# Kernel optimization log

Hardware: AMD Instinct MI355X
Metric: run time of the kernel (lower is better)

## Reference

```python
import jax, jax.numpy as jnp
import numpy as np
import math

N_HEADS = 12
HEAD_DIM = 64
D_MODEL = 768
BATCH = 2
SEQ = 2048
GRID = 46  # num_patches_per_side


def _rope_1d(x, pos, dim):
    # x: (B,S,H,dim), pos: (S,) int -> rotary embedding along last dim
    inv_freq = 1.0 / (10000.0 ** (jnp.arange(0, dim, 2, dtype=jnp.float32) / dim))  # (dim/2,)
    ang = pos.astype(jnp.float32)[:, None] * inv_freq  # (S, dim/2)
    cos = jnp.concatenate([jnp.cos(ang), jnp.cos(ang)], axis=-1)[None, :, None, :]
    sin = jnp.concatenate([jnp.sin(ang), jnp.sin(ang)], axis=-1)[None, :, None, :]
    x1, x2 = jnp.split(x, 2, axis=-1)
    rot = jnp.concatenate([-x2, x1], axis=-1)
    return x * cos.astype(x.dtype) + rot * sin.astype(x.dtype)


def _rope_2d(x, row_ids, col_ids):
    # 2D RoPE: first half of head_dim rotated by row position, second half by column position
    half = x.shape[-1] // 2
    xr = _rope_1d(x[..., :half], row_ids, half)
    xc = _rope_1d(x[..., half:], col_ids, half)
    return jnp.concatenate([xr, xc], axis=-1)


def setup_inputs() -> dict:
    key = jax.random.key(0)
    ks = jax.random.split(key, 7)
    scale = 1.0 / math.sqrt(D_MODEL)
    return {
        "x": jax.random.normal(ks[0], (BATCH, SEQ, D_MODEL), dtype=jnp.float32),
        "row_ids": jax.random.randint(ks[1], (SEQ,), 0, GRID),
        "col_ids": jax.random.randint(ks[2], (SEQ,), 0, GRID),
        "Wq": jax.random.normal(ks[3], (D_MODEL, D_MODEL), dtype=jnp.float32) * scale,
        "Wk": jax.random.normal(ks[4], (D_MODEL, D_MODEL), dtype=jnp.float32) * scale,
        "Wv": jax.random.normal(ks[5], (D_MODEL, D_MODEL), dtype=jnp.float32) * scale,
        "Wo": jax.random.normal(ks[6], (D_MODEL, D_MODEL), dtype=jnp.float32) * scale,
    }


def reference(x, row_ids, col_ids, Wq, Wk, Wv, Wo):
    B, S, _ = x.shape
    # projections (nn.Linear: y = x @ W.T)
    q = (x @ Wq.T).reshape(B, S, N_HEADS, HEAD_DIM)
    k = (x @ Wk.T).reshape(B, S, N_HEADS, HEAD_DIM)
    v = (x @ Wv.T).reshape(B, S, N_HEADS, HEAD_DIM)
    q = _rope_2d(q, row_ids, col_ids)
    k = _rope_2d(k, row_ids, col_ids)
    # (B,H,S,D)
    q = q.transpose(0, 2, 1, 3)
    k = k.transpose(0, 2, 1, 3)
    v = v.transpose(0, 2, 1, 3)
    scale = 1.0 / math.sqrt(HEAD_DIM)
    scores = jnp.einsum('bhqd,bhkd->bhqk', q, k) * scale  # (B,H,S,S)
    causal = jnp.triu(jnp.ones((S, S), dtype=bool), k=1)
    scores = jnp.where(causal, -jnp.inf, scores)
    attn = jax.nn.softmax(scores, axis=-1)
    out = jnp.einsum('bhqk,bhkd->bhqd', attn, v)
    out = out.transpose(0, 2, 1, 3).reshape(B, S, D_MODEL)
    return out @ Wo.T
```

## Files before the change

### kernel.cpp

```cpp
#include <hip/hip_runtime.h>
#include <stdint.h>
#include <stddef.h>

#define DEV __device__ __forceinline__

typedef unsigned short u16;
typedef __attribute__((ext_vector_type(8))) __bf16 bf16x8;
typedef __attribute__((ext_vector_type(4))) float f32x4;
typedef __attribute__((ext_vector_type(8))) unsigned short u16x8;
typedef __attribute__((ext_vector_type(4))) unsigned short u16x4;

DEV u16 f2bf(float f) {
  uint32_t u = __builtin_bit_cast(uint32_t, f);
  u += 0x7fffu + ((u >> 16) & 1u);
  return (u16)(u >> 16);
}
DEV float bf2f(u16 h) {
  uint32_t u = ((uint32_t)h) << 16;
  return __builtin_bit_cast(float, u);
}
DEV f32x4 mfma16(bf16x8 a, bf16x8 b, f32x4 c) {
  return __builtin_amdgcn_mfma_f32_16x16x32_bf16(a, b, c, 0, 0, 0);
}
DEV void ld_lds16(const void* g, void* l) {
  __builtin_amdgcn_global_load_lds((const __attribute__((address_space(1))) void*)g,
                                   (__attribute__((address_space(3))) void*)l, 16, 0, 0);
}

__global__ __launch_bounds__(256) void k_cvt_all(const float* __restrict__ x,
                                                 const float* __restrict__ wq,
                                                 const float* __restrict__ wk,
                                                 const float* __restrict__ wv,
                                                 const float* __restrict__ wo,
                                                 u16* __restrict__ dx,
                                                 u16* __restrict__ dqkv,
                                                 u16* __restrict__ dwo) {
  const int bid = blockIdx.x;
  const float* src;
  u16* dst;
  int off;
  if (bid < 3072) {
    src = x; dst = dx; off = bid;
  } else {
    const int t = bid - 3072;
    const int w = t / 576;
    off = t - w * 576;
    src = (w == 0) ? wq : (w == 1) ? wk : (w == 2) ? wv : wo;
    dst = (w < 3) ? (dqkv + (size_t)w * 589824) : dwo;
  }
  const int i = (off * 256 + threadIdx.x) * 4;
  const float4 f = *(const float4*)(src + i);
  u16x4 o;
  o.x = f2bf(f.x); o.y = f2bf(f.y); o.z = f2bf(f.z); o.w = f2bf(f.w);
  *(u16x4*)(dst + i) = o;
}

template <bool OUT_F32>
__global__ __launch_bounds__(256) void k_gemm_bt(const u16* __restrict__ A,
                                                 const u16* __restrict__ B,
                                                 void* __restrict__ Cv,
                                                 int N, int K) {
  __shared__ __align__(16) u16 sA[128 * 64];
  __shared__ __align__(16) u16 sB[128 * 64];
  const int tid = threadIdx.x;
  const int lane = tid & 63;
  const int wid = tid >> 6;
  const int wm = wid & 1, wn = wid >> 1;
  const int col16 = lane & 15, quad = lane >> 4;
  const int rowBase = blockIdx.y * 128;
  const int colBase = blockIdx.x * 128;
  const int seg_r = lane >> 3;
  const int seg_c = lane & 7;

  f32x4 zero; zero[0] = zero[1] = zero[2] = zero[3] = 0.0f;
  f32x4 acc[4][4];
#pragma unroll
  for (int i = 0; i < 4; ++i)
#pragma unroll
    for (int j = 0; j < 4; ++j) acc[i][j] = zero;

  for (int k0 = 0; k0 < K; k0 += 64) {
#pragma unroll
    for (int c = 0; c < 4; ++c) {
      const int seg = wid * 4 + c;
      ld_lds16(A + (size_t)(rowBase + seg * 8 + seg_r) * K + k0 + seg_c * 8, sA + seg * 512);
      ld_lds16(B + (size_t)(colBase + seg * 8 + seg_r) * K + k0 + seg_c * 8, sB + seg * 512);
    }
    __syncthreads();
#pragma unroll
    for (int kk = 0; kk < 2; ++kk) {
      bf16x8 af[4], bfr[4];
#pragma unroll
      for (int t = 0; t < 4; ++t) {
        af[t]  = *(const bf16x8*)(sA + (wm * 64 + t * 16 + col16) * 64 + kk * 32 + quad * 8);
        bfr[t] = *(const bf16x8*)(sB + (wn * 64 + t * 16 + col16) * 64 + kk * 32 + quad * 8);
      }
#pragma unroll
      for (int tm = 0; tm < 4; ++tm)
#pragma unroll
        for (int tn = 0; tn < 4; ++tn)
          acc[tm][tn] = mfma16(af[tm], bfr[tn], acc[tm][tn]);
    }
    __syncthreads();
  }

#pragma unroll
  for (int tm = 0; tm < 4; ++tm)
#pragma unroll
    for (int tn = 0; tn < 4; ++tn)
#pragma unroll
      for (int r = 0; r < 4; ++r) {
        const int row = rowBase + wm * 64 + tm * 16 + quad * 4 + r;
        const int col = colBase + wn * 64 + tn * 16 + col16;
        const float v = acc[tm][tn][r];
        if (OUT_F32) ((float*)Cv)[(size_t)row * N + col] = v;
        else         ((u16*)Cv)[(size_t)row * N + col] = f2bf(v);
      }
}

__global__ __launch_bounds__(256, 3) void k_gemm_o(const u16* __restrict__ A,
                                                   const u16* __restrict__ B,
                                                   float* __restrict__ C,
                                                   int N, int K) {
  __shared__ __align__(16) u16 sA[64 * 72];
  __shared__ __align__(16) u16 sB[64 * 72];
  const int tid = threadIdx.x;
  const int lane = tid & 63;
  const int wid = tid >> 6;
  const int col16 = lane & 15, quad = lane >> 4;
  const int wm = wid & 1, wn = wid >> 1;
  const int rowBase = blockIdx.y * 64;
  const int colBase = blockIdx.x * 64;
  const int sr = tid >> 3;
  const int sc8 = (tid & 7) * 8;

  f32x4 zero; zero[0] = zero[1] = zero[2] = zero[3] = 0.0f;
  f32x4 acc[2][2];
  acc[0][0] = zero; acc[0][1] = zero; acc[1][0] = zero; acc[1][1] = zero;

  u16x8 ar[2], br[2];
  auto gload = [&](int k0) {
    ar[0] = *(const u16x8*)(A + (size_t)(rowBase + sr) * K + k0 + sc8);
    ar[1] = *(const u16x8*)(A + (size_t)(rowBase + 32 + sr) * K + k0 + sc8);
    br[0] = *(const u16x8*)(B + (size_t)(colBase + sr) * K + k0 + sc8);
    br[1] = *(const u16x8*)(B + (size_t)(colBase + 32 + sr) * K + k0 + sc8);
  };

  gload(0);
  for (int k0 = 0; k0 < K; k0 += 64) {
    __syncthreads();
    *(u16x8*)&sA[sr * 72 + sc8] = ar[0];
    *(u16x8*)&sA[(32 + sr) * 72 + sc8] = ar[1];
    *(u16x8*)&sB[sr * 72 + sc8] = br[0];
    *(u16x8*)&sB[(32 + sr) * 72 + sc8] = br[1];
    if (k0 + 64 < K) gload(k0 + 64);
    __syncthreads();
#pragma unroll
    for (int kk = 0; kk < 2; ++kk) {
      bf16x8 af[2], bfr[2];
#pragma unroll
      for (int t = 0; t < 2; ++t) {
        af[t]  = *(const bf16x8*)&sA[(wm * 32 + t * 16 + col16) * 72 + kk * 32 + quad * 8];
        bfr[t] = *(const bf16x8*)&sB[(wn * 32 + t * 16 + col16) * 72 + kk * 32 + quad * 8];
      }
#pragma unroll
      for (int tm = 0; tm < 2; ++tm)
#pragma unroll
        for (int tn = 0; tn < 2; ++tn)
          acc[tm][tn] = mfma16(af[tm], bfr[tn], acc[tm][tn]);
    }
  }

#pragma unroll
  for (int tm = 0; tm < 2; ++tm)
#pragma unroll
    for (int tn = 0; tn < 2; ++tn)
#pragma unroll
      for (int r = 0; r < 4; ++r) {
        const int row = rowBase + wm * 32 + tm * 16 + quad * 4 + r;
        const int col = colBase + wn * 32 + tn * 16 + col16;
        C[(size_t)row * N + col] = acc[tm][tn][r];
      }
}

__global__ __launch_bounds__(256) void k_rope_vtrans(const u16* __restrict__ QKV,
                                                     const int* __restrict__ row_ids,
                                                     const int* __restrict__ col_ids,
                                                     u16* __restrict__ Qh,
                                                     u16* __restrict__ Kh,
                                                     u16* __restrict__ Vt) {
  __shared__ __align__(16) u16 tile[64][72];
  if (blockIdx.x < 6144) {
    const int t = blockIdx.x * 256 + threadIdx.x;
    const int p = t & 31;
    const int rest = t >> 5;
    const int h = rest % 12;
    const int bs = rest / 12;
    const int s = bs & 2047;
    const int b = bs >> 11;
    const int f = p & 15;
    const int hs = p >> 4;
    const int pos = hs ? col_ids[s] : row_ids[s];
    const float ang = (float)pos * expf(-(float)f * 0.5756462732485114f);
    float sn, cs;
    sincosf(ang, &sn, &cs);
    const int d1 = hs * 32 + f;
    const int d2 = d1 + 16;
    const size_t ibase = (size_t)bs * 2304 + h * 64;
    const size_t obase = (((size_t)b * 12 + h) * 2048 + s) * 64;
    {
      const float x1 = bf2f(QKV[ibase + d1]);
      const float x2 = bf2f(QKV[ibase + d2]);
      Qh[obase + d1] = f2bf(x1 * cs - x2 * sn);
      Qh[obase + d2] = f2bf(x2 * cs + x1 * sn);
    }
    {
      const float x1 = bf2f(QKV[ibase + 768 + d1]);
      const float x2 = bf2f(QKV[ibase + 768 + d2]);
      Kh[obase + d1] = f2bf(x1 * cs - x2 * sn);
      Kh[obase + d2] = f2bf(x2 * cs + x1 * sn);
    }
  } else {
    const int vb = blockIdx.x - 6144;
    const int s0 = (vb & 31) * 64;
    const int bh = vb >> 5;
    const int b = bh / 12, h = bh % 12;
    const int tid = threadIdx.x;
    const int rl = tid >> 2;
    const int cb = (tid & 3) * 16;
    const u16* src = QKV + ((size_t)b * 2048 + s0 + rl) * 2304 + 1536 + h * 64 + cb;
    const u16x8 v0 = *(const u16x8*)src;
    const u16x8 v1 = *(const u16x8*)(src + 8);
    *(u16x8*)&tile[rl][cb] = v0;
    *(u16x8*)&tile[rl][cb + 8] = v1;
    __syncthreads();
    u16x8 o0, o1;
#pragma unroll
    for (int j = 0; j < 8; ++j) {
      o0[j] = tile[cb + j][rl];
      o1[j] = tile[cb + 8 + j][rl];
    }
    u16* dst = Vt + ((size_t)bh * 64 + rl) * 2048 + s0 + cb;
    *(u16x8*)dst = o0;
    *(u16x8*)(dst + 8) = o1;
  }
}

__global__ __launch_bounds__(256, 3) void k_attn(const u16* __restrict__ Qh,
                                                 const u16* __restrict__ Kh,
                                                 const u16* __restrict__ Vt,
                                                 u16* __restrict__ O,
                                                 u16* __restrict__ Opart,
                                                 float* __restrict__ ml) {
  __shared__ __align__(16) u16 sK[2][64 * 72];
  __shared__ __align__(16) u16 sV[2][64 * 72];
  __shared__ __align__(16) u16 sP[4][16 * 72];
  const int tid = threadIdx.x;
  const int lane = tid & 63;
  const int wid = tid >> 6;
  const int col16 = lane & 15;
  const int quad = lane >> 4;
  const int bx = blockIdx.x;
  const int bh = bx / 80;
  const int u = bx - bh * 80;
  int qt, c;
  if (u < 8)       { qt = u; c = 0; }
  else if (u < 24) { const int t = u - 8;  qt = 8 + (t >> 1); c = t & 1; }
  else if (u < 48) { const int t = u - 24; const int q3 = t / 3; qt = 16 + q3; c = t - q3 * 3; }
  else             { const int t = u - 48; qt = 24 + (t >> 2); c = t & 3; }
  const int nc = (qt >> 3) + 1;
  const int tile0 = c * 8;
  const int tileE = min(tile0 + 8, qt + 1);
  const int ntiles = tileE - tile0;
  const int b = bh / 12, h = bh % 12;
  const int qw = qt * 64 + wid * 16;

  const u16* Qb = Qh + (size_t)bh * (2048 * 64);
  const u16* Kb = Kh + (size_t)bh * (2048 * 64);
  const u16* Vb = Vt + (size_t)bh * (64 * 2048);

  const bf16x8 bQ0 = *(const bf16x8*)(Qb + (size_t)(qw + col16) * 64 + quad * 8);
  const bf16x8 bQ1 = *(const bf16x8*)(Qb + (size_t)(qw + col16) * 64 + 32 + quad * 8);

  f32x4 zero; zero[0] = zero[1] = zero[2] = zero[3] = 0.0f;
  f32x4 o[4];
#pragma unroll
  for (int i = 0; i < 4; ++i) o[i] = zero;
  float m_r = -1e30f, l_r = 0.0f;

  u16* sPw = &sP[wid][0];

  const int sr = tid >> 3;
  const int sc8 = (tid & 7) * 8;
  u16x8 kr[2], vr[2];
  auto gload = [&](int kt) {
#pragma unroll
    for (int i = 0; i < 2; ++i) {
      kr[i] = *(const u16x8*)(Kb + (size_t)(kt + sr + i * 32) * 64 + sc8);
      vr[i] = *(const u16x8*)(Vb + (size_t)(sr + i * 32) * 2048 + kt + sc8);
    }
  };
  auto lwrite = [&](int buf) {
#pragma unroll
    for (int i = 0; i < 2; ++i) {
      *(u16x8*)&sK[buf][(sr + i * 32) * 72 + sc8] = kr[i];
      *(u16x8*)&sV[buf][(sr + i * 32) * 72 + sc8] = vr[i];
    }
  };

  gload(tile0 * 64);
  lwrite(0);
  if (ntiles > 1) gload((tile0 + 1) * 64);
  __syncthreads();

  for (int ki = 0; ki < ntiles; ++ki) {
    const int buf = ki & 1;
    const int kt = (tile0 + ki) * 64;
    if (ki + 1 < ntiles) {
      lwrite(buf ^ 1);
      if (ki + 2 < ntiles) gload((tile0 + ki + 2) * 64);
    }
    bf16x8 ka0[4], ka1[4];
#pragma unroll
    for (int tn = 0; tn < 4; ++tn) {
      const int base = (tn * 16 + col16) * 72 + quad * 8;
      ka0[tn] = *(const bf16x8*)&sK[buf][base];
      ka1[tn] = *(const bf16x8*)&sK[buf][base + 32];
    }
    f32x4 sc[4];
#pragma unroll
    for (int tn = 0; tn < 4; ++tn)
      sc[tn] = mfma16(ka1[tn], bQ1, mfma16(ka0[tn], bQ0, zero));
    bf16x8 va0[4], va1[4];
#pragma unroll
    for (int tn = 0; tn < 4; ++tn) {
      const int base = (tn * 16 + col16) * 72 + quad * 8;
      va0[tn] = *(const bf16x8*)&sV[buf][base];
      va1[tn] = *(const bf16x8*)&sV[buf][base + 32];
    }
    if (kt + 63 > qw) {
#pragma unroll
      for (int tn = 0; tn < 4; ++tn)
#pragma unroll
        for (int rr = 0; rr < 4; ++rr) {
          float v = sc[tn][rr] * 0.125f;
          if (kt + tn * 16 + quad * 4 + rr > qw + col16) v = -1e30f;
          sc[tn][rr] = v;
        }
    } else {
#pragma unroll
      for (int tn = 0; tn < 4; ++tn)
#pragma unroll
        for (int rr = 0; rr < 4; ++rr) sc[tn][rr] *= 0.125f;
    }
    float vm = sc[0][0];
#pragma unroll
    for (int tn = 0; tn < 4; ++tn)
#pragma unroll
      for (int rr = 0; rr < 4; ++rr) vm = fmaxf(vm, sc[tn][rr]);
    vm = fmaxf(vm, __shfl_xor(vm, 16, 64));
    vm = fmaxf(vm, __shfl_xor(vm, 32, 64));
    const float mn = fmaxf(m_r, vm);
    const float alpha = __expf(m_r - mn);
    m_r = mn;
    float rs = 0.0f;
#pragma unroll
    for (int tn = 0; tn < 4; ++tn)
#pragma unroll
      for (int h2 = 0; h2 < 2; ++h2) {
        const float p0 = __expf(sc[tn][2 * h2] - mn);
        const float p1 = __expf(sc[tn][2 * h2 + 1] - mn);
        rs += p0 + p1;
        const uint32_t w = (uint32_t)f2bf(p0) | ((uint32_t)f2bf(p1) << 16);
        ((uint32_t*)sPw)[col16 * 36 + tn * 8 + quad * 2 + h2] = w;
      }
    rs += __shfl_xor(rs, 16, 64);
    rs += __shfl_xor(rs, 32, 64);
    l_r = l_r * alpha + rs;
#pragma unroll
    for (int t = 0; t < 4; ++t)
#pragma unroll
      for (int rr = 0; rr < 4; ++rr) o[t][rr] *= alpha;
    asm volatile("s_waitcnt lgkmcnt(0)" ::: "memory");
    const bf16x8 bP0 = *(const bf16x8*)(sPw + col16 * 72 + quad * 8);
    const bf16x8 bP1 = *(const bf16x8*)(sPw + col16 * 72 + 32 + quad * 8);
#pragma unroll
    for (int tn = 0; tn < 4; ++tn)
      o[tn] = mfma16(va1[tn], bP1, mfma16(va0[tn], bP0, o[tn]));
    __syncthreads();
  }

  if (nc == 1) {
    const float invl = 1.0f / l_r;
    const size_t row = (size_t)b * 2048 + qw + col16;
#pragma unroll
    for (int tn = 0; tn < 4; ++tn)
#pragma unroll
      for (int h2 = 0; h2 < 2; ++h2) {
        const float v0 = o[tn][2 * h2] * invl;
        const float v1 = o[tn][2 * h2 + 1] * invl;
        const uint32_t w = (uint32_t)f2bf(v0) | ((uint32_t)f2bf(v1) << 16);
        const int col = h * 64 + tn * 16 + quad * 4 + 2 * h2;
        *(uint32_t*)(O + row * 768 + col) = w;
      }
  } else {
    u16* op = Opart + (size_t)bx * 4096 + (wid * 16 + col16) * 64;
#pragma unroll
    for (int tn = 0; tn < 4; ++tn)
#pragma unroll
      for (int h2 = 0; h2 < 2; ++h2) {
        const uint32_t w = (uint32_t)f2bf(o[tn][2 * h2]) | ((uint32_t)f2bf(o[tn][2 * h2 + 1]) << 16);
        *(uint32_t*)(op + tn * 16 + quad * 4 + 2 * h2) = w;
      }
    if (quad == 0) {
      float* mlp = ml + (size_t)bx * 128;
      mlp[wid * 16 + col16] = m_r;
      mlp[64 + wid * 16 + col16] = l_r;
    }
  }
}

__global__ __launch_bounds__(256) void k_combine(const u16* __restrict__ Opart,
                                                 const float* __restrict__ ml,
                                                 u16* __restrict__ O) {
  const int bx = blockIdx.x;
  const int bh = bx / 24;
  const int qt = 8 + (bx - bh * 24);
  const int b = bh / 12, h = bh % 12;
  const int nc = (qt >> 3) + 1;
  const int prefix = (qt < 16) ? (8 + 2 * (qt - 8))
                   : (qt < 24) ? (24 + 3 * (qt - 16))
                               : (48 + 4 * (qt - 24));
  const int slot0 = bh * 80 + prefix;
  const int tid = threadIdx.x;
  const int r = tid >> 2;
  const int d0 = (tid & 3) * 16;

  float m_i[4], w_i[4];
  float M = -1e30f;
  for (int i = 0; i < nc; ++i) {
    m_i[i] = ml[(size_t)(slot0 + i) * 128 + r];
    M = fmaxf(M, m_i[i]);
  }
  float l = 0.0f;
  for (int i = 0; i < nc; ++i) {
    w_i[i] = __expf(m_i[i] - M);
    l += w_i[i] * ml[(size_t)(slot0 + i) * 128 + 64 + r];
  }
  const float invl = 1.0f / l;

  float a[16];
#pragma unroll
  for (int j = 0; j < 16; ++j) a[j] = 0.0f;
  for (int i = 0; i < nc; ++i) {
    const u16* op = Opart + (size_t)(slot0 + i) * 4096 + r * 64 + d0;
    const u16x8 v0 = *(const u16x8*)op;
    const u16x8 v1 = *(const u16x8*)(op + 8);
#pragma unroll
    for (int j = 0; j < 8; ++j) {
      a[j] += w_i[i] * bf2f(v0[j]);
      a[8 + j] += w_i[i] * bf2f(v1[j]);
    }
  }
  u16x8 o0, o1;
#pragma unroll
  for (int j = 0; j < 8; ++j) {
    o0[j] = f2bf(a[j] * invl);
    o1[j] = f2bf(a[8 + j] * invl);
  }
  u16* dst = O + (size_t)(b * 2048 + qt * 64 + r) * 768 + h * 64 + d0;
  *(u16x8*)dst = o0;
  *(u16x8*)(dst + 8) = o1;
}

extern "C" void kernel_launch(void* const* d_in, const int* in_sizes, int n_in,
                              void* d_out, int out_size, void* d_ws, size_t ws_size,
                              hipStream_t stream) {
  const float* x       = (const float*)d_in[0];
  const int*   row_ids = (const int*)d_in[1];
  const int*   col_ids = (const int*)d_in[2];
  const float* Wq      = (const float*)d_in[3];
  const float* Wk      = (const float*)d_in[4];
  const float* Wv      = (const float*)d_in[5];
  const float* Wo      = (const float*)d_in[6];
  float* out = (float*)d_out;

  uint8_t* w8 = (uint8_t*)d_ws;
  u16* x_bf = (u16*)(w8 + 0);
  u16* wqkv = (u16*)(w8 + 6291456);
  u16* wo   = (u16*)(w8 + 9830400);
  u16* qkv  = (u16*)(w8 + 11010048);
  u16* qh   = (u16*)(w8 + 29884416);
  u16* kh   = (u16*)(w8 + 36175872);
  u16* vt   = (u16*)(w8 + 42467328);
  u16* obuf = (u16*)(w8 + 48758784);
  u16*   opart = (u16*)(w8 + 11010048);
  float* mlbuf = (float*)(w8 + 11010048 + 15728640);

  k_cvt_all<<<5376, 256, 0, stream>>>(x, Wq, Wk, Wv, Wo, x_bf, wqkv, wo);
  k_gemm_bt<false><<<dim3(18, 32), 256, 0, stream>>>(x_bf, wqkv, (void*)qkv, 2304, 768);
  k_rope_vtrans<<<6912, 256, 0, stream>>>(qkv, row_ids, col_ids, qh, kh, vt);
  k_attn<<<1920, 256, 0, stream>>>(qh, kh, vt, obuf, opart, mlbuf);
  k_combine<<<576, 256, 0, stream>>>(opart, mlbuf, obuf);
  k_gemm_o<<<dim3(12, 64), 256, 0, stream>>>(obuf, wo, out, 768, 768);
}
```

Measured before the change: 190.0 us.

## Fuse RoPE and V transpose into QKV GEMM epilogue, fold softmax scale into Q

The QKV projection GEMM now applies 2D RoPE in its epilogue and writes Q and K directly in head-major layout, with V written transposed. This removes the intermediate QKV buffer and the separate rope/transpose kernel launch. Q is pre-scaled by 1/sqrt(d)*log2(e), so attention uses exp2 and drops the per-score multiply. Probabilities are truncated to bf16 rather than rounded, and the row sum is taken over the truncated values. The costs are more scattered 16-bit stores in the epilogue and a small change in rounding behaviour.

```diff
diff --git a/kernel.cpp b/kernel.cpp
--- a/kernel.cpp
+++ b/kernel.cpp
@@ -26,6 +26,8 @@
   __builtin_amdgcn_global_load_lds((const __attribute__((address_space(1))) void*)g,
                                    (__attribute__((address_space(3))) void*)l, 16, 0, 0);
 }
+
+#define Q_SCALE 0.18033688011112042f
 
 __global__ __launch_bounds__(256) void k_cvt_all(const float* __restrict__ x,
                                                  const float* __restrict__ wq,
@@ -55,13 +57,17 @@
   *(u16x4*)(dst + i) = o;
 }
 
-template <bool OUT_F32>
-__global__ __launch_bounds__(256) void k_gemm_bt(const u16* __restrict__ A,
-                                                 const u16* __restrict__ B,
-                                                 void* __restrict__ Cv,
-                                                 int N, int K) {
+__global__ __launch_bounds__(256) void k_gemm_qkv(const u16* __restrict__ A,
+                                                  const u16* __restrict__ B,
+                                                  const int* __restrict__ row_ids,
+                                                  const int* __restrict__ col_ids,
+                                                  u16* __restrict__ Qh,
+                                                  u16* __restrict__ Kh,
+                                                  u16* __restrict__ Vt) {
+  const int K = 768;
   __shared__ __align__(16) u16 sA[128 * 64];
   __shared__ __align__(16) u16 sB[128 * 64];
+  __shared__ int sIds[256];
   const int tid = threadIdx.x;
   const int lane = tid & 63;
   const int wid = tid >> 6;
@@ -104,18 +110,52 @@
     __syncthreads();
   }
 
-#pragma unroll
-  for (int tm = 0; tm < 4; ++tm)
-#pragma unroll
-    for (int tn = 0; tn < 4; ++tn)
+  const int bx = blockIdx.x;
+  const int type = bx / 6;
+  const int h = (bx % 6) * 2 + wn;
+  const int bb = rowBase >> 11;
+  const int s0 = rowBase & 2047;
+  const size_t bh = (size_t)bb * 12 + h;
+
+  if (type < 2) {
+    if (tid < 128) {
+      sIds[tid] = row_ids[s0 + tid];
+      sIds[128 + tid] = col_ids[s0 + tid];
+    }
+    __syncthreads();
+    u16* dst = (type == 0) ? Qh : Kh;
+    const float scl = (type == 0) ? Q_SCALE : 1.0f;
+    const float invf = exp2f(-(float)col16 * 0.8304820237218406f);
+#pragma unroll
+    for (int tm = 0; tm < 4; ++tm)
 #pragma unroll
       for (int r = 0; r < 4; ++r) {
-        const int row = rowBase + wm * 64 + tm * 16 + quad * 4 + r;
-        const int col = colBase + wn * 64 + tn * 16 + col16;
-        const float v = acc[tm][tn][r];
-        if (OUT_F32) ((float*)Cv)[(size_t)row * N + col] = v;
-        else         ((u16*)Cv)[(size_t)row * N + col] = f2bf(v);
-      }
+        const int lrow = wm * 64 + tm * 16 + quad * 4 + r;
+        const float aR = (float)sIds[lrow] * invf;
+        const float aC = (float)sIds[128 + lrow] * invf;
+        const float cR = __cosf(aR), sR = __sinf(aR);
+        const float cC = __cosf(aC), sC = __sinf(aC);
+        const float x1 = acc[tm][0][r], x2 = acc[tm][1][r];
+        const float x3 = acc[tm][2][r], x4 = acc[tm][3][r];
+        u16* p = dst + (bh * 2048 + s0 + lrow) * 64;
+        p[col16]      = f2bf((x1 * cR - x2 * sR) * scl);
+        p[col16 + 16] = f2bf((x2 * cR + x1 * sR) * scl);
+        p[col16 + 32] = f2bf((x3 * cC - x4 * sC) * scl);
+        p[col16 + 48] = f2bf((x4 * cC + x3 * sC) * scl);
+      }
+  } else {
+#pragma unroll
+    for (int tm = 0; tm < 4; ++tm)
+#pragma unroll
+      for (int tn = 0; tn < 4; ++tn) {
+        const int d = tn * 16 + col16;
+        const int srow = s0 + wm * 64 + tm * 16 + quad * 4;
+        u16x4 o4;
+#pragma unroll
+        for (int r = 0; r < 4; ++r) o4[r] = f2bf(acc[tm][tn][r]);
+        *(u16x4*)(Vt + (bh * 64 + d) * 2048 + srow) = o4;
+      }
+  }
 }
 
 __global__ __launch_bounds__(256, 3) void k_gemm_o(const u16* __restrict__ A,
@@ -181,69 +221,6 @@
         const int col = colBase + wn * 32 + tn * 16 + col16;
         C[(size_t)row * N + col] = acc[tm][tn][r];
       }
-}
-
-__global__ __launch_bounds__(256) void k_rope_vtrans(const u16* __restrict__ QKV,
-                                                     const int* __restrict__ row_ids,
-                                                     const int* __restrict__ col_ids,
-                                                     u16* __restrict__ Qh,
-                                                     u16* __restrict__ Kh,
-                                                     u16* __restrict__ Vt) {
-  __shared__ __align__(16) u16 tile[64][72];
-  if (blockIdx.x < 6144) {
-    const int t = blockIdx.x * 256 + threadIdx.x;
-    const int p = t & 31;
-    const int rest = t >> 5;
-    const int h = rest % 12;
-    const int bs = rest / 12;
-    const int s = bs & 2047;
-    const int b = bs >> 11;
-    const int f = p & 15;
-    const int hs = p >> 4;
-    const int pos = hs ? col_ids[s] : row_ids[s];
-    const float ang = (float)pos * expf(-(float)f * 0.5756462732485114f);
-    float sn, cs;
-    sincosf(ang, &sn, &cs);
-    const int d1 = hs * 32 + f;
-    const int d2 = d1 + 16;
-    const size_t ibase = (size_t)bs * 2304 + h * 64;
-    const size_t obase = (((size_t)b * 12 + h) * 2048 + s) * 64;
-    {
-      const float x1 = bf2f(QKV[ibase + d1]);
-      const float x2 = bf2f(QKV[ibase + d2]);
-      Qh[obase + d1] = f2bf(x1 * cs - x2 * sn);
-      Qh[obase + d2] = f2bf(x2 * cs + x1 * sn);
-    }
-    {
-      const float x1 = bf2f(QKV[ibase + 768 + d1]);
-      const float x2 = bf2f(QKV[ibase + 768 + d2]);
-      Kh[obase + d1] = f2bf(x1 * cs - x2 * sn);
-      Kh[obase + d2] = f2bf(x2 * cs + x1 * sn);
-    }
-  } else {
-    const int vb = blockIdx.x - 6144;
-    const int s0 = (vb & 31) * 64;
-    const int bh = vb >> 5;
-    const int b = bh / 12, h = bh % 12;
-    const int tid = threadIdx.x;
-    const int rl = tid >> 2;
-    const int cb = (tid & 3) * 16;
-    const u16* src = QKV + ((size_t)b * 2048 + s0 + rl) * 2304 + 1536 + h * 64 + cb;
-    const u16x8 v0 = *(const u16x8*)src;
-    const u16x8 v1 = *(const u16x8*)(src + 8);
-    *(u16x8*)&tile[rl][cb] = v0;
-    *(u16x8*)&tile[rl][cb + 8] = v1;
-    __syncthreads();
-    u16x8 o0, o1;
-#pragma unroll
-    for (int j = 0; j < 8; ++j) {
-      o0[j] = tile[cb + j][rl];
-      o1[j] = tile[cb + 8 + j][rl];
-    }
-    u16* dst = Vt + ((size_t)bh * 64 + rl) * 2048 + s0 + cb;
-    *(u16x8*)dst = o0;
-    *(u16x8*)(dst + 8) = o1;
-  }
 }
 
 __global__ __launch_bounds__(256, 3) void k_attn(const u16* __restrict__ Qh,
@@ -342,16 +319,8 @@
 #pragma unroll
       for (int tn = 0; tn < 4; ++tn)
 #pragma unroll
-        for (int rr = 0; rr < 4; ++rr) {
-          float v = sc[tn][rr] * 0.125f;
-          if (kt + tn * 16 + quad * 4 + rr > qw + col16) v = -1e30f;
-          sc[tn][rr] = v;
-        }
-    } else {
-#pragma unroll
-      for (int tn = 0; tn < 4; ++tn)
-#pragma unroll
-        for (int rr = 0; rr < 4; ++rr) sc[tn][rr] *= 0.125f;
+        for (int rr = 0; rr < 4; ++rr)
+          if (kt + tn * 16 + quad * 4 + rr > qw + col16) sc[tn][rr] = -1e30f;
     }
     float vm = sc[0][0];
 #pragma unroll
@@ -361,18 +330,19 @@
     vm = fmaxf(vm, __shfl_xor(vm, 16, 64));
     vm = fmaxf(vm, __shfl_xor(vm, 32, 64));
     const float mn = fmaxf(m_r, vm);
-    const float alpha = __expf(m_r - mn);
+    const float alpha = exp2f(m_r - mn);
     m_r = mn;
     float rs = 0.0f;
 #pragma unroll
     for (int tn = 0; tn < 4; ++tn)
 #pragma unroll
       for (int h2 = 0; h2 < 2; ++h2) {
-        const float p0 = __expf(sc[tn][2 * h2] - mn);
-        const float p1 = __expf(sc[tn][2 * h2 + 1] - mn);
-        rs += p0 + p1;
-        const uint32_t w = (uint32_t)f2bf(p0) | ((uint32_t)f2bf(p1) << 16);
-        ((uint32_t*)sPw)[col16 * 36 + tn * 8 + quad * 2 + h2] = w;
+        const float p0 = exp2f(sc[tn][2 * h2] - mn);
+        const float p1 = exp2f(sc[tn][2 * h2 + 1] - mn);
+        const uint32_t u0 = __builtin_bit_cast(uint32_t, p0) & 0xffff0000u;
+        const uint32_t u1 = __builtin_bit_cast(uint32_t, p1) & 0xffff0000u;
+        rs += __builtin_bit_cast(float, u0) + __builtin_bit_cast(float, u1);
+        ((uint32_t*)sPw)[col16 * 36 + tn * 8 + quad * 2 + h2] = u1 | (u0 >> 16);
       }
     rs += __shfl_xor(rs, 16, 64);
     rs += __shfl_xor(rs, 32, 64);
@@ -444,7 +414,7 @@
   }
   float l = 0.0f;
   for (int i = 0; i < nc; ++i) {
-    w_i[i] = __expf(m_i[i] - M);
+    w_i[i] = exp2f(m_i[i] - M);
     l += w_i[i] * ml[(size_t)(slot0 + i) * 128 + 64 + r];
   }
   const float invl = 1.0f / l;
@@ -489,7 +459,6 @@
   u16* x_bf = (u16*)(w8 + 0);
   u16* wqkv = (u16*)(w8 + 6291456);
   u16* wo   = (u16*)(w8 + 9830400);
-  u16* qkv  = (u16*)(w8 + 11010048);
   u16* qh   = (u16*)(w8 + 29884416);
   u16* kh   = (u16*)(w8 + 36175872);
   u16* vt   = (u16*)(w8 + 42467328);
@@ -498,8 +467,7 @@
   float* mlbuf = (float*)(w8 + 11010048 + 15728640);
 
   k_cvt_all<<<5376, 256, 0, stream>>>(x, Wq, Wk, Wv, Wo, x_bf, wqkv, wo);
-  k_gemm_bt<false><<<dim3(18, 32), 256, 0, stream>>>(x_bf, wqkv, (void*)qkv, 2304, 768);
-  k_rope_vtrans<<<6912, 256, 0, stream>>>(qkv, row_ids, col_ids, qh, kh, vt);
+  k_gemm_qkv<<<dim3(18, 32), 256, 0, stream>>>(x_bf, wqkv, row_ids, col_ids, qh, kh, vt);
   k_attn<<<1920, 256, 0, stream>>>(qh, kh, vt, obuf, opart, mlbuf);
   k_combine<<<576, 256, 0, stream>>>(opart, mlbuf, obuf);
   k_gemm_o<<<dim3(12, 64), 256, 0, stream>>>(obuf, wo, out, 768, 768);
```

After: 184.0 us. 3.2% less time.
